# Kernel optimization log

Hardware: AMD Instinct MI355X
Metric: run time of the kernel (lower is better)

The kernel has to match this reference:

```python
import jax, jax.numpy as jnp
import numpy as np

N_NODES = 100000
N_EDGES = 1600000
N_GRAPHS = 256
IN_C = 64
HID = 128
OUT = 128
BN_EPS = 1e-5


def setup_inputs() -> dict:
    key = jax.random.key(0)
    ks = jax.random.split(key, 24)
    x = jax.random.normal(ks[0], (N_NODES, IN_C), jnp.float32)
    edge_index = jax.random.randint(ks[1], (2, N_EDGES), 0, N_NODES, dtype=jnp.int64 if jax.config.jax_enable_x64 else jnp.int32)
    batch = jnp.sort(jax.random.randint(ks[2], (N_NODES,), 0, N_GRAPHS))

    def lin(k, i, o):
        return (jax.random.normal(k, (i, o), jnp.float32) / np.float32(np.sqrt(i)))

    d = {"x": x, "edge_index": edge_index, "batch": batch}
    in_dims = [IN_C, HID, HID]
    for l in range(3):
        d[f"w1_{l}"] = lin(ks[3 + 6 * l], in_dims[l], HID)
        d[f"b1_{l}"] = jnp.zeros((HID,), jnp.float32)
        d[f"w2_{l}"] = lin(ks[4 + 6 * l], HID, HID)
        d[f"b2_{l}"] = jnp.zeros((HID,), jnp.float32)
        d[f"gamma_{l}"] = jnp.ones((HID,), jnp.float32)
        d[f"beta_{l}"] = jnp.zeros((HID,), jnp.float32)
    d["proj_w"] = lin(ks[22], HID, OUT)
    d["proj_b"] = jnp.zeros((OUT,), jnp.float32)
    return d


def _gin_forward(x, edge_index, batch, layers, proj_w, proj_b):
    src, dst = edge_index[0], edge_index[1]
    h = x
    for (w1, b1, w2, b2, g, b) in layers:
        # GINConv (eps=0, aggr='add'): MLP(h_i + sum_{j->i} h_j)
        agg = jax.ops.segment_sum(h[src], dst, num_segments=h.shape[0])
        z = h + agg
        z = jax.nn.relu(z @ w1 + b1) @ w2 + b2
        # BatchNorm1d, training mode (biased batch stats)
        mean = z.mean(axis=0)
        var = z.var(axis=0)
        z = (z - mean) * jax.lax.rsqrt(var + BN_EPS) * g + b
        h = jax.nn.relu(z)
    # global_mean_pool over graph ids
    s = jax.ops.segment_sum(h, batch, num_segments=N_GRAPHS)
    cnt = jax.ops.segment_sum(jnp.ones((h.shape[0], 1), h.dtype), batch, num_segments=N_GRAPHS)
    hg = s / jnp.maximum(cnt, 1.0)
    return hg @ proj_w + proj_b


def reference(x, edge_index, batch,
              w1_0, b1_0, w2_0, b2_0, gamma_0, beta_0,
              w1_1, b1_1, w2_1, b2_1, gamma_1, beta_1,
              w1_2, b1_2, w2_2, b2_2, gamma_2, beta_2,
              proj_w, proj_b):
    layers = [
        (w1_0, b1_0, w2_0, b2_0, gamma_0, beta_0),
        (w1_1, b1_1, w2_1, b2_1, gamma_1, beta_1),
        (w1_2, b1_2, w2_2, b2_2, gamma_2, beta_2),
    ]
    return _gin_forward(x, edge_index, batch, layers, proj_w, proj_b)
```

## Files before the change

### kernel.cpp

```cpp
#include <hip/hip_runtime.h>

#define N_NODES 100000
#define N_EDGES 1600000
#define N_GRAPHS 256
#define HID 128
#define BN_EPS 1e-5f

#define NT 1563
#define EB 4096
#define RB 391
#define MB 1563

typedef __bf16 bf16x8 __attribute__((ext_vector_type(8)));
typedef __bf16 bf16x4 __attribute__((ext_vector_type(4)));
typedef __bf16 bf16x2 __attribute__((ext_vector_type(2)));
typedef float f32x4 __attribute__((ext_vector_type(4)));

__global__ __launch_bounds__(256) void prep_all_kernel(
    const float* __restrict__ wa, const float* __restrict__ wb,
    const float* __restrict__ wc, const float* __restrict__ wd,
    const float* __restrict__ we, const float* __restrict__ wf,
    __bf16* __restrict__ wt) {
  int idx = blockIdx.x * 256 + threadIdx.x;
  if (idx >= 90112) return;
  const float* w;
  int K, local;
  if (idx < 8192) { w = wa; K = 64; local = idx; }
  else {
    int s = (idx - 8192) / 16384;
    local = (idx - 8192) - s * 16384;
    K = 128;
    w = (s == 0) ? wb : (s == 1) ? wc : (s == 2) ? wd : (s == 3) ? we : wf;
  }
  int n = local / K, k = local - n * K;
  wt[idx] = (__bf16)w[k * 128 + n];
}

__global__ __launch_bounds__(256) void x_convert_kernel(const float* __restrict__ x,
                                                        __bf16* __restrict__ xb) {
  int idx = blockIdx.x * 256 + threadIdx.x;
  if (idx >= N_NODES * 16) return;
  f32x4 v = ((const f32x4*)x)[idx];
  bf16x4 o = {(__bf16)v[0], (__bf16)v[1], (__bf16)v[2], (__bf16)v[3]};
  ((bf16x4*)xb)[idx] = o;
}

__global__ __launch_bounds__(256) void tile_hist_kernel(const int* __restrict__ ei,
                                                        int* __restrict__ tcnt) {
  __shared__ int hist[NT];
  int t = threadIdx.x;
  for (int i = t; i < NT; i += 256) hist[i] = 0;
  __syncthreads();
  int base = blockIdx.x * EB;
#pragma unroll 4
  for (int i = 0; i < EB / 256; i++) {
    int e = base + i * 256 + t;
    if (e < N_EDGES) atomicAdd(&hist[ei[N_EDGES + e] >> 6], 1);
  }
  __syncthreads();
  for (int i = t; i < NT; i += 256) {
    int h = hist[i];
    if (h) atomicAdd(&tcnt[i], h);
  }
}

__global__ __launch_bounds__(256) void tile_scan_kernel(const int* __restrict__ tcnt,
                                                        int* __restrict__ tstart,
                                                        int* __restrict__ gcursor) {
  __shared__ int ps[256];
  int t = threadIdx.x;
  const int CH = (NT + 255) / 256;
  int lo = t * CH, hi = min(lo + CH, NT);
  int s = 0;
  for (int i = lo; i < hi; i++) s += tcnt[i];
  ps[t] = s;
  __syncthreads();
  for (int off = 1; off < 256; off <<= 1) {
    int v = ps[t];
    int u = (t >= off) ? ps[t - off] : 0;
    __syncthreads();
    ps[t] = v + u;
    __syncthreads();
  }
  int base = (t == 0) ? 0 : ps[t - 1];
  for (int i = lo; i < hi; i++) {
    tstart[i] = base;
    gcursor[i] = base;
    base += tcnt[i];
  }
  if (t == 0) tstart[NT] = N_EDGES;
}

__global__ __launch_bounds__(256) void reorder2_kernel(const int* __restrict__ ei,
                                                       int* __restrict__ gcursor,
                                                       int* __restrict__ epack) {
  __shared__ int hist[NT];
  int t = threadIdx.x;
  for (int i = t; i < NT; i += 256) hist[i] = 0;
  __syncthreads();
  int base = blockIdx.x * EB;
#pragma unroll 4
  for (int i = 0; i < EB / 256; i++) {
    int e = base + i * 256 + t;
    if (e < N_EDGES) atomicAdd(&hist[ei[N_EDGES + e] >> 6], 1);
  }
  __syncthreads();
  for (int i = t; i < NT; i += 256) {
    int h = hist[i];
    if (h) hist[i] = atomicAdd(&gcursor[i], h);
  }
  __syncthreads();
#pragma unroll 4
  for (int i = 0; i < EB / 256; i++) {
    int e = base + i * 256 + t;
    if (e < N_EDGES) {
      int d = ei[N_EDGES + e];
      int s = ei[e];
      int pos = atomicAdd(&hist[d >> 6], 1);
      epack[pos] = (s << 6) | (d & 63);
    }
  }
}

__global__ __launch_bounds__(256) void row_sort_kernel(const int* __restrict__ tstart,
                                                       const int* __restrict__ epack,
                                                       int* __restrict__ starts,
                                                       int* __restrict__ srcs) {
  __shared__ int cnt[64];
  __shared__ int rbase[65];
  __shared__ int rofs[64];
  int t = threadIdx.x, b = blockIdx.x;
  int ts = tstart[b], te = tstart[b + 1];
  if (t < 64) cnt[t] = 0;
  __syncthreads();
  for (int i = ts + t; i < te; i += 256) atomicAdd(&cnt[epack[i] & 63], 1);
  __syncthreads();
  if (t == 0) {
    int a = 0;
    for (int r = 0; r < 64; r++) { rbase[r] = a; a += cnt[r]; }
    rbase[64] = a;
  }
  __syncthreads();
  if (t < 64) rofs[t] = ts + rbase[t];
  if (t <= 64) {
    int gr = b * 64 + t;
    if (gr <= N_NODES) starts[gr] = ts + rbase[t];
  }
  __syncthreads();
  for (int i = ts + t; i < te; i += 256) {
    int p = epack[i];
    int pos = atomicAdd(&rofs[p & 63], 1);
    srcs[pos] = p >> 6;
  }
}

template <int C, bool BN>
__global__ __launch_bounds__(256) void gather_kernel(const __bf16* __restrict__ h,
                                                     const float* __restrict__ bnab,
                                                     const int* __restrict__ starts,
                                                     const int* __restrict__ srcs,
                                                     __bf16* __restrict__ z) {
  const int lane = threadIdx.x & 63;
  const int row = blockIdx.x * 4 + (threadIdx.x >> 6);
  if (row >= N_NODES) return;
  int e0 = starts[row], e1 = starts[row + 1];
  int deg = e1 - e0;
  int idxv = srcs[min(e0 + lane, N_EDGES - 1)];
  int dcap = min(deg, 64);

  float bna0 = 0.f, bna1 = 0.f, bnb0 = 0.f, bnb1 = 0.f;
  if constexpr (BN) {
    bna0 = bnab[lane * 2];
    bna1 = bnab[lane * 2 + 1];
    bnb0 = bnab[HID + lane * 2];
    bnb1 = bnab[HID + lane * 2 + 1];
  }

#define ACCBN(vv, sx, sy)                                              \
  do {                                                                 \
    if constexpr (BN) {                                                \
      sx += fmaxf(fmaf(bna0, (float)(vv)[0], bnb0), 0.f);              \
      sy += fmaxf(fmaf(bna1, (float)(vv)[1], bnb1), 0.f);              \
    } else {                                                           \
      sx += (float)(vv)[0];                                            \
      sy += (float)(vv)[1];                                            \
    }                                                                  \
  } while (0)

  if constexpr (C == 64) {
    float acc = (float)h[(size_t)row * 64 + lane];
    float s0 = 0.f, s1 = 0.f, s2 = 0.f, s3 = 0.f, s4 = 0.f, s5 = 0.f, s6 = 0.f, s7 = 0.f;
    int j = 0;
    for (; j + 7 < dcap; j += 8) {
      int i0 = __builtin_amdgcn_readlane(idxv, j);
      int i1 = __builtin_amdgcn_readlane(idxv, j + 1);
      int i2 = __builtin_amdgcn_readlane(idxv, j + 2);
      int i3 = __builtin_amdgcn_readlane(idxv, j + 3);
      int i4 = __builtin_amdgcn_readlane(idxv, j + 4);
      int i5 = __builtin_amdgcn_readlane(idxv, j + 5);
      int i6 = __builtin_amdgcn_readlane(idxv, j + 6);
      int i7 = __builtin_amdgcn_readlane(idxv, j + 7);
      float v0 = (float)h[(size_t)i0 * 64 + lane];
      float v1 = (float)h[(size_t)i1 * 64 + lane];
      float v2 = (float)h[(size_t)i2 * 64 + lane];
      float v3 = (float)h[(size_t)i3 * 64 + lane];
      float v4 = (float)h[(size_t)i4 * 64 + lane];
      float v5 = (float)h[(size_t)i5 * 64 + lane];
      float v6 = (float)h[(size_t)i6 * 64 + lane];
      float v7 = (float)h[(size_t)i7 * 64 + lane];
      s0 += v0; s1 += v1; s2 += v2; s3 += v3;
      s4 += v4; s5 += v5; s6 += v6; s7 += v7;
    }
    for (; j < dcap; j++) {
      int i0 = __builtin_amdgcn_readlane(idxv, j);
      s0 += (float)h[(size_t)i0 * 64 + lane];
    }
    for (int e = e0 + 64; e < e1; e++) s0 += (float)h[(size_t)srcs[e] * 64 + lane];
    acc += ((s0 + s1) + (s2 + s3)) + ((s4 + s5) + (s6 + s7));
    z[(size_t)row * 64 + lane] = (__bf16)acc;
  } else {
    bf16x2 sv = *(const bf16x2*)(h + (size_t)row * 128 + lane * 2);
    float ax = 0.f, ay = 0.f;
    ACCBN(sv, ax, ay);
    float2 s0 = {0.f, 0.f}, s1 = {0.f, 0.f}, s2 = {0.f, 0.f}, s3 = {0.f, 0.f};
    float2 s4 = {0.f, 0.f}, s5 = {0.f, 0.f}, s6 = {0.f, 0.f}, s7 = {0.f, 0.f};
    int j = 0;
    for (; j + 7 < dcap; j += 8) {
      int i0 = __builtin_amdgcn_readlane(idxv, j);
      int i1 = __builtin_amdgcn_readlane(idxv, j + 1);
      int i2 = __builtin_amdgcn_readlane(idxv, j + 2);
      int i3 = __builtin_amdgcn_readlane(idxv, j + 3);
      int i4 = __builtin_amdgcn_readlane(idxv, j + 4);
      int i5 = __builtin_amdgcn_readlane(idxv, j + 5);
      int i6 = __builtin_amdgcn_readlane(idxv, j + 6);
      int i7 = __builtin_amdgcn_readlane(idxv, j + 7);
      bf16x2 v0 = *(const bf16x2*)(h + (size_t)i0 * 128 + lane * 2);
      bf16x2 v1 = *(const bf16x2*)(h + (size_t)i1 * 128 + lane * 2);
      bf16x2 v2 = *(const bf16x2*)(h + (size_t)i2 * 128 + lane * 2);
      bf16x2 v3 = *(const bf16x2*)(h + (size_t)i3 * 128 + lane * 2);
      bf16x2 v4 = *(const bf16x2*)(h + (size_t)i4 * 128 + lane * 2);
      bf16x2 v5 = *(const bf16x2*)(h + (size_t)i5 * 128 + lane * 2);
      bf16x2 v6 = *(const bf16x2*)(h + (size_t)i6 * 128 + lane * 2);
      bf16x2 v7 = *(const bf16x2*)(h + (size_t)i7 * 128 + lane * 2);
      ACCBN(v0, s0.x, s0.y);
      ACCBN(v1, s1.x, s1.y);
      ACCBN(v2, s2.x, s2.y);
      ACCBN(v3, s3.x, s3.y);
      ACCBN(v4, s4.x, s4.y);
      ACCBN(v5, s5.x, s5.y);
      ACCBN(v6, s6.x, s6.y);
      ACCBN(v7, s7.x, s7.y);
    }
    for (; j < dcap; j++) {
      int i0 = __builtin_amdgcn_readlane(idxv, j);
      bf16x2 vv = *(const bf16x2*)(h + (size_t)i0 * 128 + lane * 2);
      ACCBN(vv, s0.x, s0.y);
    }
    for (int e = e0 + 64; e < e1; e++) {
      bf16x2 vv = *(const bf16x2*)(h + (size_t)srcs[e] * 128 + lane * 2);
      ACCBN(vv, s0.x, s0.y);
    }
    ax += ((s0.x + s1.x) + (s2.x + s3.x)) + ((s4.x + s5.x) + (s6.x + s7.x));
    ay += ((s0.y + s1.y) + (s2.y + s3.y)) + ((s4.y + s5.y) + (s6.y + s7.y));
    bf16x2 z2 = {(__bf16)ax, (__bf16)ay};
    *(bf16x2*)(z + (size_t)row * 128 + lane * 2) = z2;
  }
#undef ACCBN
}

template <int CIN>
__global__ __launch_bounds__(256) void mlp_kernel(
    const __bf16* __restrict__ z, const __bf16* __restrict__ w1t,
    const float* __restrict__ b1, const __bf16* __restrict__ w2t,
    const float* __restrict__ b2, __bf16* __restrict__ u,
    float* __restrict__ part) {
  constexpr int TS = HID + 8;
  __shared__ __align__(16) __bf16 sm[64 * TS];

  const int t = threadIdx.x;
  const int wave = t >> 6;
  const int lane = t & 63;
  const int l16 = lane & 15;
  const int quad = lane >> 4;
  const int rowbase = blockIdx.x * 64;
  const int nvalid = min(64, N_NODES - rowbase);
  const int arow = min(rowbase + wave * 16 + l16, N_NODES - 1);

  const f32x4 zero4 = {0.f, 0.f, 0.f, 0.f};
  f32x4 acc[8];

  {
    bf16x8 af[CIN / 32];
    const __bf16* ap = z + (size_t)arow * CIN + quad * 8;
#pragma unroll
    for (int ks = 0; ks < CIN / 32; ks++) af[ks] = *(const bf16x8*)(ap + ks * 32);
#pragma unroll
    for (int ct = 0; ct < 8; ct++) acc[ct] = zero4;
#pragma unroll
    for (int ks = 0; ks < CIN / 32; ks++) {
#pragma unroll
      for (int ct = 0; ct < 8; ct++) {
        bf16x8 bfr = *(const bf16x8*)(w1t + (ct * 16 + l16) * CIN + ks * 32 + quad * 8);
        acc[ct] = __builtin_amdgcn_mfma_f32_16x16x32_bf16(af[ks], bfr, acc[ct], 0, 0, 0);
      }
    }
#pragma unroll
    for (int ct = 0; ct < 8; ct++) {
      int col = ct * 16 + l16;
      float bias = b1[col];
#pragma unroll
      for (int r = 0; r < 4; r++) {
        float v = acc[ct][r] + bias;
        sm[(wave * 16 + quad * 4 + r) * TS + col] = (__bf16)(v > 0.f ? v : 0.f);
      }
    }
  }

  {
#pragma unroll
    for (int ct = 0; ct < 8; ct++) acc[ct] = zero4;
    const __bf16* arowp = sm + (wave * 16 + l16) * TS + quad * 8;
#pragma unroll
    for (int ks = 0; ks < HID / 32; ks++) {
      bf16x8 af = *(const bf16x8*)(arowp + ks * 32);
#pragma unroll
      for (int ct = 0; ct < 8; ct++) {
        bf16x8 bfr = *(const bf16x8*)(w2t + (ct * 16 + l16) * HID + ks * 32 + quad * 8);
        acc[ct] = __builtin_amdgcn_mfma_f32_16x16x32_bf16(af, bfr, acc[ct], 0, 0, 0);
      }
    }
#pragma unroll
    for (int ct = 0; ct < 8; ct++) {
      int col = ct * 16 + l16;
      float bias = b2[col];
#pragma unroll
      for (int r = 0; r < 4; r++) {
        sm[(wave * 16 + quad * 4 + r) * TS + col] = (__bf16)(acc[ct][r] + bias);
      }
    }
  }
  __syncthreads();

  for (int f = t; f < 64 * 16; f += 256) {
    int r = f >> 4, c8 = f & 15;
    if (r < nvalid) {
      bf16x8 v = *(const bf16x8*)(sm + r * TS + c8 * 8);
      *(bf16x8*)(u + (size_t)(rowbase + r) * HID + c8 * 8) = v;
    }
  }
  if (t < HID) {
    float s = 0.f, sq = 0.f;
    for (int r = 0; r < nvalid; r++) {
      float v = (float)sm[r * TS + t];
      s += v;
      sq += v * v;
    }
    part[(size_t)blockIdx.x * 256 + t] = s;
    part[(size_t)blockIdx.x * 256 + HID + t] = sq;
  }
}

__global__ __launch_bounds__(256) void bn_stats_kernel(const float* __restrict__ part,
                                                       const float* __restrict__ gamma,
                                                       const float* __restrict__ beta,
                                                       float* __restrict__ bnab) {
  __shared__ float ss[256], qq[256];
  int c = blockIdx.x;
  int t = threadIdx.x;
  float s = 0.f, q = 0.f;
  for (int b = t; b < MB; b += 256) {
    s += part[(size_t)b * 256 + c];
    q += part[(size_t)b * 256 + HID + c];
  }
  ss[t] = s; qq[t] = q;
  __syncthreads();
  for (int off = 128; off > 0; off >>= 1) {
    if (t < off) { ss[t] += ss[t + off]; qq[t] += qq[t + off]; }
    __syncthreads();
  }
  if (t == 0) {
    const float invN = 1.f / (float)N_NODES;
    float mean = ss[0] * invN;
    float var = qq[0] * invN - mean * mean;
    float a = gamma[c] * rsqrtf(var + BN_EPS);
    bnab[c] = a;
    bnab[HID + c] = beta[c] - mean * a;
  }
}

__global__ __launch_bounds__(128) void bn_apply_pool_kernel(const __bf16* __restrict__ u,
                                                            const float* __restrict__ bnab,
                                                            const int* __restrict__ batch,
                                                            float* __restrict__ pool) {
  int c = threadIdx.x;
  int r0 = blockIdx.x * 64;
  if (r0 >= N_NODES) return;
  int rend = min(r0 + 64, N_NODES);
  float a = bnab[c], b = bnab[HID + c];
  float accv = 0.f;
  int curg = -1;
  for (int r = r0; r < rend; r++) {
    int g = batch[r];
    if (g != curg) {
      if (curg >= 0) atomicAdd(&pool[curg * HID + c], accv);
      curg = g;
      accv = 0.f;
    }
    float v = (float)u[(size_t)r * HID + c];
    v = v * a + b;
    accv += (v > 0.f ? v : 0.f);
  }
  if (curg >= 0) atomicAdd(&pool[curg * HID + c], accv);
}

__global__ __launch_bounds__(256) void count_kernel(const int* __restrict__ batch,
                                                    int* __restrict__ counts) {
  int t = blockIdx.x * 256 + threadIdx.x;
  int r0 = t * 64;
  if (r0 >= N_NODES) return;
  int rend = min(r0 + 64, N_NODES);
  int curg = batch[r0], cnt = 0;
  for (int r = r0; r < rend; r++) {
    int g = batch[r];
    if (g != curg) {
      atomicAdd(&counts[curg], cnt);
      curg = g;
      cnt = 1;
    } else {
      cnt++;
    }
  }
  atomicAdd(&counts[curg], cnt);
}

__global__ __launch_bounds__(128) void pool_proj_kernel(const float* __restrict__ pool,
                                                        const int* __restrict__ counts,
                                                        const float* __restrict__ pw,
                                                        const float* __restrict__ pb,
                                                        float* __restrict__ out) {
  int g = blockIdx.x;
  int c = threadIdx.x;
  __shared__ float hg[HID];
  float cnt = (float)max(counts[g], 1);
  hg[c] = pool[g * HID + c] / cnt;
  __syncthreads();
  float acc = pb[c];
#pragma unroll 8
  for (int k = 0; k < HID; k++) acc += hg[k] * pw[k * HID + c];
  out[g * HID + c] = acc;
}

extern "C" void kernel_launch(void* const* d_in, const int* in_sizes, int n_in,
                              void* d_out, int out_size, void* d_ws, size_t ws_size,
                              hipStream_t stream) {
  (void)in_sizes; (void)n_in; (void)out_size; (void)ws_size;
  const float* x = (const float*)d_in[0];
  const int* ei = (const int*)d_in[1];
  const int* batch = (const int*)d_in[2];
  const float* w1[3] = {(const float*)d_in[3], (const float*)d_in[9], (const float*)d_in[15]};
  const float* b1[3] = {(const float*)d_in[4], (const float*)d_in[10], (const float*)d_in[16]};
  const float* w2[3] = {(const float*)d_in[5], (const float*)d_in[11], (const float*)d_in[17]};
  const float* b2[3] = {(const float*)d_in[6], (const float*)d_in[12], (const float*)d_in[18]};
  const float* gm[3] = {(const float*)d_in[7], (const float*)d_in[13], (const float*)d_in[19]};
  const float* bt[3] = {(const float*)d_in[8], (const float*)d_in[14], (const float*)d_in[20]};
  const float* pw = (const float*)d_in[21];
  const float* pb = (const float*)d_in[22];
  float* out = (float*)d_out;

  char* ws = (char*)d_ws;
  __bf16* bufA = (__bf16*)ws;        ws += (size_t)N_NODES * HID * 2;
  __bf16* bufB = (__bf16*)ws;        ws += (size_t)N_NODES * HID * 2;
  __bf16* bufC = (__bf16*)ws;        ws += (size_t)N_NODES * HID * 2;
  __bf16* z0 = (__bf16*)ws;          ws += (size_t)N_NODES * 64 * 2;
  __bf16* xb = (__bf16*)ws;          ws += (size_t)N_NODES * 64 * 2;
  int* srcs = (int*)ws;              ws += (size_t)N_EDGES * 4;
  int* epack = (int*)ws;             ws += (size_t)N_EDGES * 4;
  int* starts = (int*)ws;            ws += (size_t)(N_NODES + 1) * 4;
  int* tcnt = (int*)ws;              ws += NT * 4;
  int* tstart = (int*)ws;            ws += (NT + 1) * 4;
  int* gcursor = (int*)ws;           ws += NT * 4;
  ws = (char*)(((uintptr_t)ws + 63) & ~(uintptr_t)63);
  float* part = (float*)ws;          ws += (size_t)MB * 256 * 4;
  __bf16* wt_all = (__bf16*)ws;      ws += 90112 * 2;
  ws = (char*)(((uintptr_t)ws + 63) & ~(uintptr_t)63);
  float* bnab = (float*)ws;          ws += 256 * 4;
  float* pool = (float*)ws;          ws += N_GRAPHS * HID * 4;
  int* counts = (int*)ws;            ws += N_GRAPHS * 4;

  __bf16* w1t0 = wt_all;
  __bf16* w2t0 = wt_all + 8192;
  __bf16* w1t1 = wt_all + 24576;
  __bf16* w2t1 = wt_all + 40960;
  __bf16* w1t2 = wt_all + 57344;
  __bf16* w2t2 = wt_all + 73728;

  const int gat_blocks = (N_NODES + 3) / 4;

  prep_all_kernel<<<(90112 + 255) / 256, 256, 0, stream>>>(
      w1[0], w2[0], w1[1], w2[1], w1[2], w2[2], wt_all);
  x_convert_kernel<<<(N_NODES * 16 + 255) / 256, 256, 0, stream>>>(x, xb);

  hipMemsetAsync(tcnt, 0, NT * 4, stream);
  tile_hist_kernel<<<RB, 256, 0, stream>>>(ei, tcnt);
  tile_scan_kernel<<<1, 256, 0, stream>>>(tcnt, tstart, gcursor);
  reorder2_kernel<<<RB, 256, 0, stream>>>(ei, gcursor, epack);
  row_sort_kernel<<<NT, 256, 0, stream>>>(tstart, epack, starts, srcs);

  hipMemsetAsync(pool, 0, (size_t)N_GRAPHS * HID * 4 + N_GRAPHS * 4, stream);
  count_kernel<<<((N_NODES + 63) / 64 + 255) / 256, 256, 0, stream>>>(batch, counts);

  gather_kernel<64, false><<<gat_blocks, 256, 0, stream>>>(xb, nullptr, starts, srcs, z0);
  mlp_kernel<64><<<MB, 256, 0, stream>>>(z0, w1t0, b1[0], w2t0, b2[0], bufA, part);
  bn_stats_kernel<<<HID, 256, 0, stream>>>(part, gm[0], bt[0], bnab);

  gather_kernel<128, true><<<gat_blocks, 256, 0, stream>>>(bufA, bnab, starts, srcs, bufC);
  mlp_kernel<128><<<MB, 256, 0, stream>>>(bufC, w1t1, b1[1], w2t1, b2[1], bufB, part);
  bn_stats_kernel<<<HID, 256, 0, stream>>>(part, gm[1], bt[1], bnab);

  gather_kernel<128, true><<<gat_blocks, 256, 0, stream>>>(bufB, bnab, starts, srcs, bufC);
  mlp_kernel<128><<<MB, 256, 0, stream>>>(bufC, w1t2, b1[2], w2t2, b2[2], bufA, part);
  bn_stats_kernel<<<HID, 256, 0, stream>>>(part, gm[2], bt[2], bnab);

  bn_apply_pool_kernel<<<MB, 128, 0, stream>>>(bufA, bnab, batch, pool);

  pool_proj_kernel<<<N_GRAPHS, 128, 0, stream>>>(pool, counts, pw, pb, out);
}
```

Measured before the change: 594.6 us.

## Split gather wavefronts into two half-waves over edges and merge setup kernels

The gather kernel now has each 64-lane wavefront process two neighbor edges at once. Each half-wave loads a full feature row using wider per-lane loads (bf16x4 for 128 channels, bf16x2 for 64), and the two halves are combined with a cross-half shuffle at the end. The aim is to raise memory-level parallelism and request width on the irregular neighbor gathers. Separately, x conversion, weight transpose and graph counting are fused into one setup kernel to cut launch overhead. The cost is extra tail handling for odd degrees and a shuffle reduction, with half the lanes idle during the final write.

```diff
diff --git a/kernel.cpp b/kernel.cpp
--- a/kernel.cpp
+++ b/kernel.cpp
@@ -16,33 +16,52 @@
 typedef __bf16 bf16x2 __attribute__((ext_vector_type(2)));
 typedef float f32x4 __attribute__((ext_vector_type(4)));
 
-__global__ __launch_bounds__(256) void prep_all_kernel(
+__global__ __launch_bounds__(256) void setup_kernel(
+    const float* __restrict__ x, __bf16* __restrict__ xb,
     const float* __restrict__ wa, const float* __restrict__ wb,
     const float* __restrict__ wc, const float* __restrict__ wd,
     const float* __restrict__ we, const float* __restrict__ wf,
-    __bf16* __restrict__ wt) {
-  int idx = blockIdx.x * 256 + threadIdx.x;
-  if (idx >= 90112) return;
-  const float* w;
-  int K, local;
-  if (idx < 8192) { w = wa; K = 64; local = idx; }
-  else {
-    int s = (idx - 8192) / 16384;
-    local = (idx - 8192) - s * 16384;
-    K = 128;
-    w = (s == 0) ? wb : (s == 1) ? wc : (s == 2) ? wd : (s == 3) ? we : wf;
-  }
-  int n = local / K, k = local - n * K;
-  wt[idx] = (__bf16)w[k * 128 + n];
-}
-
-__global__ __launch_bounds__(256) void x_convert_kernel(const float* __restrict__ x,
-                                                        __bf16* __restrict__ xb) {
-  int idx = blockIdx.x * 256 + threadIdx.x;
-  if (idx >= N_NODES * 16) return;
-  f32x4 v = ((const f32x4*)x)[idx];
-  bf16x4 o = {(__bf16)v[0], (__bf16)v[1], (__bf16)v[2], (__bf16)v[3]};
-  ((bf16x4*)xb)[idx] = o;
+    __bf16* __restrict__ wt,
+    const int* __restrict__ batch, int* __restrict__ counts) {
+  int b = blockIdx.x;
+  if (b < 6250) {
+    int idx = b * 256 + threadIdx.x;
+    if (idx >= N_NODES * 16) return;
+    f32x4 v = ((const f32x4*)x)[idx];
+    bf16x4 o = {(__bf16)v[0], (__bf16)v[1], (__bf16)v[2], (__bf16)v[3]};
+    ((bf16x4*)xb)[idx] = o;
+  } else if (b < 6250 + 352) {
+    int idx = (b - 6250) * 256 + threadIdx.x;
+    if (idx >= 90112) return;
+    const float* w;
+    int K, local;
+    if (idx < 8192) { w = wa; K = 64; local = idx; }
+    else {
+      int s = (idx - 8192) / 16384;
+      local = (idx - 8192) - s * 16384;
+      K = 128;
+      w = (s == 0) ? wb : (s == 1) ? wc : (s == 2) ? wd : (s == 3) ? we : wf;
+    }
+    int n = local / K, k = local - n * K;
+    wt[idx] = (__bf16)w[k * 128 + n];
+  } else {
+    int t = (b - 6602) * 256 + threadIdx.x;
+    int r0 = t * 64;
+    if (r0 >= N_NODES) return;
+    int rend = min(r0 + 64, N_NODES);
+    int curg = batch[r0], cnt = 0;
+    for (int r = r0; r < rend; r++) {
+      int g = batch[r];
+      if (g != curg) {
+        atomicAdd(&counts[curg], cnt);
+        curg = g;
+        cnt = 1;
+      } else {
+        cnt++;
+      }
+    }
+    atomicAdd(&counts[curg], cnt);
+  }
 }
 
 __global__ __launch_bounds__(256) void tile_hist_kernel(const int* __restrict__ ei,
@@ -161,6 +180,8 @@
                                                      const int* __restrict__ srcs,
                                                      __bf16* __restrict__ z) {
   const int lane = threadIdx.x & 63;
+  const int half = lane >> 5;
+  const int fl = lane & 31;
   const int row = blockIdx.x * 4 + (threadIdx.x >> 6);
   if (row >= N_NODES) return;
   int e0 = starts[row], e1 = starts[row + 1];
@@ -168,104 +189,131 @@
   int idxv = srcs[min(e0 + lane, N_EDGES - 1)];
   int dcap = min(deg, 64);
 
-  float bna0 = 0.f, bna1 = 0.f, bnb0 = 0.f, bnb1 = 0.f;
-  if constexpr (BN) {
-    bna0 = bnab[lane * 2];
-    bna1 = bnab[lane * 2 + 1];
-    bnb0 = bnab[HID + lane * 2];
-    bnb1 = bnab[HID + lane * 2 + 1];
-  }
-
-#define ACCBN(vv, sx, sy)                                              \
-  do {                                                                 \
-    if constexpr (BN) {                                                \
-      sx += fmaxf(fmaf(bna0, (float)(vv)[0], bnb0), 0.f);              \
-      sy += fmaxf(fmaf(bna1, (float)(vv)[1], bnb1), 0.f);              \
-    } else {                                                           \
-      sx += (float)(vv)[0];                                            \
-      sy += (float)(vv)[1];                                            \
-    }                                                                  \
-  } while (0)
-
-  if constexpr (C == 64) {
-    float acc = (float)h[(size_t)row * 64 + lane];
-    float s0 = 0.f, s1 = 0.f, s2 = 0.f, s3 = 0.f, s4 = 0.f, s5 = 0.f, s6 = 0.f, s7 = 0.f;
+  if constexpr (C == 128) {
+    f32x4 a4, b4;
+    if constexpr (BN) {
+      a4 = *(const f32x4*)(bnab + fl * 4);
+      b4 = *(const f32x4*)(bnab + HID + fl * 4);
+    }
+#define ACC4(vv, ss)                                                   \
+    do {                                                               \
+      if constexpr (BN) {                                              \
+        ss[0] += fmaxf(fmaf(a4[0], (float)(vv)[0], b4[0]), 0.f);       \
+        ss[1] += fmaxf(fmaf(a4[1], (float)(vv)[1], b4[1]), 0.f);       \
+        ss[2] += fmaxf(fmaf(a4[2], (float)(vv)[2], b4[2]), 0.f);       \
+        ss[3] += fmaxf(fmaf(a4[3], (float)(vv)[3], b4[3]), 0.f);       \
+      } else {                                                         \
+        ss[0] += (float)(vv)[0]; ss[1] += (float)(vv)[1];              \
+        ss[2] += (float)(vv)[2]; ss[3] += (float)(vv)[3];              \
+      }                                                                \
+    } while (0)
+    f32x4 sa[4] = {};
     int j = 0;
-    for (; j + 7 < dcap; j += 8) {
-      int i0 = __builtin_amdgcn_readlane(idxv, j);
-      int i1 = __builtin_amdgcn_readlane(idxv, j + 1);
-      int i2 = __builtin_amdgcn_readlane(idxv, j + 2);
-      int i3 = __builtin_amdgcn_readlane(idxv, j + 3);
-      int i4 = __builtin_amdgcn_readlane(idxv, j + 4);
-      int i5 = __builtin_amdgcn_readlane(idxv, j + 5);
-      int i6 = __builtin_amdgcn_readlane(idxv, j + 6);
-      int i7 = __builtin_amdgcn_readlane(idxv, j + 7);
-      float v0 = (float)h[(size_t)i0 * 64 + lane];
-      float v1 = (float)h[(size_t)i1 * 64 + lane];
-      float v2 = (float)h[(size_t)i2 * 64 + lane];
-      float v3 = (float)h[(size_t)i3 * 64 + lane];
-      float v4 = (float)h[(size_t)i4 * 64 + lane];
-      float v5 = (float)h[(size_t)i5 * 64 + lane];
-      float v6 = (float)h[(size_t)i6 * 64 + lane];
-      float v7 = (float)h[(size_t)i7 * 64 + lane];
-      s0 += v0; s1 += v1; s2 += v2; s3 += v3;
-      s4 += v4; s5 += v5; s6 += v6; s7 += v7;
-    }
-    for (; j < dcap; j++) {
-      int i0 = __builtin_amdgcn_readlane(idxv, j);
-      s0 += (float)h[(size_t)i0 * 64 + lane];
-    }
-    for (int e = e0 + 64; e < e1; e++) s0 += (float)h[(size_t)srcs[e] * 64 + lane];
-    acc += ((s0 + s1) + (s2 + s3)) + ((s4 + s5) + (s6 + s7));
-    z[(size_t)row * 64 + lane] = (__bf16)acc;
+    for (; j + 15 < dcap; j += 16) {
+      int idx[8];
+#pragma unroll
+      for (int k = 0; k < 8; k++) {
+        int p = __builtin_amdgcn_readlane(idxv, j + 2 * k);
+        int q = __builtin_amdgcn_readlane(idxv, j + 2 * k + 1);
+        idx[k] = half ? q : p;
+      }
+      bf16x4 vv[8];
+#pragma unroll
+      for (int k = 0; k < 8; k++)
+        vv[k] = *(const bf16x4*)(h + (size_t)idx[k] * 128 + fl * 4);
+#pragma unroll
+      for (int k = 0; k < 8; k++) ACC4(vv[k], sa[k & 3]);
+    }
+    for (; j + 1 < dcap; j += 2) {
+      int p = __builtin_amdgcn_readlane(idxv, j);
+      int q = __builtin_amdgcn_readlane(idxv, j + 1);
+      int ik = half ? q : p;
+      bf16x4 vv = *(const bf16x4*)(h + (size_t)ik * 128 + fl * 4);
+      ACC4(vv, sa[0]);
+    }
+    if (j < dcap) {
+      int p = __builtin_amdgcn_readlane(idxv, j);
+      bf16x4 vv = *(const bf16x4*)(h + (size_t)p * 128 + fl * 4);
+      if (half == 0) ACC4(vv, sa[0]);
+    }
+    for (int e = e0 + 64; e + 1 < e1; e += 2) {
+      int ik = srcs[e + half];
+      bf16x4 vv = *(const bf16x4*)(h + (size_t)ik * 128 + fl * 4);
+      ACC4(vv, sa[1]);
+    }
+    if (deg > 64 && ((deg - 64) & 1)) {
+      int ik = srcs[e1 - 1];
+      bf16x4 vv = *(const bf16x4*)(h + (size_t)ik * 128 + fl * 4);
+      if (half == 0) ACC4(vv, sa[1]);
+    }
+    f32x4 tot = (sa[0] + sa[1]) + (sa[2] + sa[3]);
+#pragma unroll
+    for (int i = 0; i < 4; i++) tot[i] += __shfl_xor(tot[i], 32);
+    if (half == 0) {
+      bf16x4 sv = *(const bf16x4*)(h + (size_t)row * 128 + fl * 4);
+      ACC4(sv, tot);
+      bf16x4 o = {(__bf16)tot[0], (__bf16)tot[1], (__bf16)tot[2], (__bf16)tot[3]};
+      *(bf16x4*)(z + (size_t)row * 128 + fl * 4) = o;
+    }
+#undef ACC4
   } else {
-    bf16x2 sv = *(const bf16x2*)(h + (size_t)row * 128 + lane * 2);
-    float ax = 0.f, ay = 0.f;
-    ACCBN(sv, ax, ay);
-    float2 s0 = {0.f, 0.f}, s1 = {0.f, 0.f}, s2 = {0.f, 0.f}, s3 = {0.f, 0.f};
-    float2 s4 = {0.f, 0.f}, s5 = {0.f, 0.f}, s6 = {0.f, 0.f}, s7 = {0.f, 0.f};
+    float2 sa[4] = {};
+#define ACC2(vv, ss)                                                   \
+    do {                                                               \
+      ss.x += (float)(vv)[0];                                          \
+      ss.y += (float)(vv)[1];                                          \
+    } while (0)
     int j = 0;
-    for (; j + 7 < dcap; j += 8) {
-      int i0 = __builtin_amdgcn_readlane(idxv, j);
-      int i1 = __builtin_amdgcn_readlane(idxv, j + 1);
-      int i2 = __builtin_amdgcn_readlane(idxv, j + 2);
-      int i3 = __builtin_amdgcn_readlane(idxv, j + 3);
-      int i4 = __builtin_amdgcn_readlane(idxv, j + 4);
-      int i5 = __builtin_amdgcn_readlane(idxv, j + 5);
-      int i6 = __builtin_amdgcn_readlane(idxv, j + 6);
-      int i7 = __builtin_amdgcn_readlane(idxv, j + 7);
-      bf16x2 v0 = *(const bf16x2*)(h + (size_t)i0 * 128 + lane * 2);
-      bf16x2 v1 = *(const bf16x2*)(h + (size_t)i1 * 128 + lane * 2);
-      bf16x2 v2 = *(const bf16x2*)(h + (size_t)i2 * 128 + lane * 2);
-      bf16x2 v3 = *(const bf16x2*)(h + (size_t)i3 * 128 + lane * 2);
-      bf16x2 v4 = *(const bf16x2*)(h + (size_t)i4 * 128 + lane * 2);
-      bf16x2 v5 = *(const bf16x2*)(h + (size_t)i5 * 128 + lane * 2);
-      bf16x2 v6 = *(const bf16x2*)(h + (size_t)i6 * 128 + lane * 2);
-      bf16x2 v7 = *(const bf16x2*)(h + (size_t)i7 * 128 + lane * 2);
-      ACCBN(v0, s0.x, s0.y);
-      ACCBN(v1, s1.x, s1.y);
-      ACCBN(v2, s2.x, s2.y);
-      ACCBN(v3, s3.x, s3.y);
-      ACCBN(v4, s4.x, s4.y);
-      ACCBN(v5, s5.x, s5.y);
-      ACCBN(v6, s6.x, s6.y);
-      ACCBN(v7, s7.x, s7.y);
-    }
-    for (; j < dcap; j++) {
-      int i0 = __builtin_amdgcn_readlane(idxv, j);
-      bf16x2 vv = *(const bf16x2*)(h + (size_t)i0 * 128 + lane * 2);
-      ACCBN(vv, s0.x, s0.y);
-    }
-    for (int e = e0 + 64; e < e1; e++) {
-      bf16x2 vv = *(const bf16x2*)(h + (size_t)srcs[e] * 128 + lane * 2);
-      ACCBN(vv, s0.x, s0.y);
-    }
-    ax += ((s0.x + s1.x) + (s2.x + s3.x)) + ((s4.x + s5.x) + (s6.x + s7.x));
-    ay += ((s0.y + s1.y) + (s2.y + s3.y)) + ((s4.y + s5.y) + (s6.y + s7.y));
-    bf16x2 z2 = {(__bf16)ax, (__bf16)ay};
-    *(bf16x2*)(z + (size_t)row * 128 + lane * 2) = z2;
-  }
-#undef ACCBN
+    for (; j + 15 < dcap; j += 16) {
+      int idx[8];
+#pragma unroll
+      for (int k = 0; k < 8; k++) {
+        int p = __builtin_amdgcn_readlane(idxv, j + 2 * k);
+        int q = __builtin_amdgcn_readlane(idxv, j + 2 * k + 1);
+        idx[k] = half ? q : p;
+      }
+      bf16x2 vv[8];
+#pragma unroll
+      for (int k = 0; k < 8; k++)
+        vv[k] = *(const bf16x2*)(h + (size_t)idx[k] * 64 + fl * 2);
+#pragma unroll
+      for (int k = 0; k < 8; k++) ACC2(vv[k], sa[k & 3]);
+    }
+    for (; j + 1 < dcap; j += 2) {
+      int p = __builtin_amdgcn_readlane(idxv, j);
+      int q = __builtin_amdgcn_readlane(idxv, j + 1);
+      int ik = half ? q : p;
+      bf16x2 vv = *(const bf16x2*)(h + (size_t)ik * 64 + fl * 2);
+      ACC2(vv, sa[0]);
+    }
+    if (j < dcap) {
+      int p = __builtin_amdgcn_readlane(idxv, j);
+      bf16x2 vv = *(const bf16x2*)(h + (size_t)p * 64 + fl * 2);
+      if (half == 0) ACC2(vv, sa[0]);
+    }
+    for (int e = e0 + 64; e + 1 < e1; e += 2) {
+      int ik = srcs[e + half];
+      bf16x2 vv = *(const bf16x2*)(h + (size_t)ik * 64 + fl * 2);
+      ACC2(vv, sa[1]);
+    }
+    if (deg > 64 && ((deg - 64) & 1)) {
+      int ik = srcs[e1 - 1];
+      bf16x2 vv = *(const bf16x2*)(h + (size_t)ik * 64 + fl * 2);
+      if (half == 0) ACC2(vv, sa[1]);
+    }
+    float tx = (sa[0].x + sa[1].x) + (sa[2].x + sa[3].x);
+    float ty = (sa[0].y + sa[1].y) + (sa[2].y + sa[3].y);
+    tx += __shfl_xor(tx, 32);
+    ty += __shfl_xor(ty, 32);
+    if (half == 0) {
+      bf16x2 sv = *(const bf16x2*)(h + (size_t)row * 64 + fl * 2);
+      tx += (float)sv[0];
+      ty += (float)sv[1];
+      bf16x2 o = {(__bf16)tx, (__bf16)ty};
+      *(bf16x2*)(z + (size_t)row * 64 + fl * 2) = o;
+    }
+#undef ACC2
+  }
 }
 
 template <int CIN>
@@ -411,26 +459,6 @@
     accv += (v > 0.f ? v : 0.f);
   }
   if (curg >= 0) atomicAdd(&pool[curg * HID + c], accv);
-}
-
-__global__ __launch_bounds__(256) void count_kernel(const int* __restrict__ batch,
-                                                    int* __restrict__ counts) {
-  int t = blockIdx.x * 256 + threadIdx.x;
-  int r0 = t * 64;
-  if (r0 >= N_NODES) return;
-  int rend = min(r0 + 64, N_NODES);
-  int curg = batch[r0], cnt = 0;
-  for (int r = r0; r < rend; r++) {
-    int g = batch[r];
-    if (g != curg) {
-      atomicAdd(&counts[curg], cnt);
-      curg = g;
-      cnt = 1;
-    } else {
-      cnt++;
-    }
-  }
-  atomicAdd(&counts[curg], cnt);
 }
 
 __global__ __launch_bounds__(128) void pool_proj_kernel(const float* __restrict__ pool,
@@ -496,19 +524,17 @@
 
   const int gat_blocks = (N_NODES + 3) / 4;
 
-  prep_all_kernel<<<(90112 + 255) / 256, 256, 0, stream>>>(
-      w1[0], w2[0], w1[1], w2[1], w1[2], w2[2], wt_all);
-  x_convert_kernel<<<(N_NODES * 16 + 255) / 256, 256, 0, stream>>>(x, xb);
-
+  hipMemsetAsync(pool, 0, (size_t)N_GRAPHS * HID * 4 + N_GRAPHS * 4, stream);
   hipMemsetAsync(tcnt, 0, NT * 4, stream);
+
+  setup_kernel<<<6609, 256, 0, stream>>>(x, xb, w1[0], w2[0], w1[1], w2[1],
+                                         w1[2], w2[2], wt_all, batch, counts);
+
   tile_hist_kernel<<<RB, 256, 0, stream>>>(ei, tcnt);
   tile_scan_kernel<<<1, 256, 0, stream>>>(tcnt, tstart, gcursor);
   reorder2_kernel<<<RB, 256, 0, stream>>>(ei, gcursor, epack);
   row_sort_kernel<<<NT, 256, 0, stream>>>(tstart, epack, starts, srcs);
 
-  hipMemsetAsync(pool, 0, (size_t)N_GRAPHS * HID * 4 + N_GRAPHS * 4, stream);
-  count_kernel<<<((N_NODES + 63) / 64 + 255) / 256, 256, 0, stream>>>(batch, counts);
-
   gather_kernel<64, false><<<gat_blocks, 256, 0, stream>>>(xb, nullptr, starts, srcs, z0);
   mlp_kernel<64><<<MB, 256, 0, stream>>>(z0, w1t0, b1[0], w2t0, b2[0], bufA, part);
   bn_stats_kernel<<<HID, 256, 0, stream>>>(part, gm[0], bt[0], bnab);
```

Measured after the change: 606.2 us. About the same (+2.0%).
